# Kernel optimization log

Hardware: AMD Instinct MI355X
Metric: run time of the kernel (lower is better)

Reference implementation:

```python
import jax, jax.numpy as jnp
import numpy as np

D_MODEL = 1024
N_HEADS = 16
HEAD_DIM = D_MODEL // N_HEADS
FFN = 4096
NUM_REL = 64
BATCH = 4
SEQ = 1024
EPS = 1e-6


def _layernorm(x, g, b):
    mu = jnp.mean(x, axis=-1, keepdims=True)
    var = jnp.mean(jnp.square(x - mu), axis=-1, keepdims=True)
    return (x - mu) * jax.lax.rsqrt(var + EPS) * g + b


def setup_inputs() -> dict:
    key = jax.random.key(0)
    ks = jax.random.split(key, 16)
    s_d = 1.0 / np.sqrt(D_MODEL)
    s_f = 1.0 / np.sqrt(FFN)
    inp = {
        "x": jax.random.normal(ks[0], (BATCH, SEQ, D_MODEL), jnp.float32),
        "relative_ids": jax.random.randint(ks[1], (SEQ, SEQ), 0, NUM_REL),
        # attention projections (row-major: y = x @ W + b)
        "Wq": jax.random.normal(ks[2], (D_MODEL, D_MODEL), jnp.float32) * s_d,
        "bq": jnp.zeros((D_MODEL,), jnp.float32),
        "Wk": jax.random.normal(ks[3], (D_MODEL, D_MODEL), jnp.float32) * s_d,
        "bk": jnp.zeros((D_MODEL,), jnp.float32),
        "Wv": jax.random.normal(ks[4], (D_MODEL, D_MODEL), jnp.float32) * s_d,
        "bv": jnp.zeros((D_MODEL,), jnp.float32),
        "Wo": jax.random.normal(ks[5], (D_MODEL, D_MODEL), jnp.float32) * s_d,
        "bo": jnp.zeros((D_MODEL,), jnp.float32),
        # relative position tables: Ek for keys (rel-e), Eb per-head bias (rel-b)
        "Ek": jax.random.normal(ks[6], (NUM_REL, HEAD_DIM), jnp.float32) * (1.0 / np.sqrt(HEAD_DIM)),
        "Eb": jax.random.normal(ks[7], (NUM_REL, N_HEADS), jnp.float32) * 0.02,
        # layernorms
        "g1": jnp.ones((D_MODEL,), jnp.float32),
        "b1": jnp.zeros((D_MODEL,), jnp.float32),
        "g2": jnp.ones((D_MODEL,), jnp.float32),
        "b2": jnp.zeros((D_MODEL,), jnp.float32),
        # FFN
        "W1": jax.random.normal(ks[8], (D_MODEL, FFN), jnp.float32) * s_d,
        "bf1": jnp.zeros((FFN,), jnp.float32),
        "W2": jax.random.normal(ks[9], (FFN, D_MODEL), jnp.float32) * s_f,
        "bf2": jnp.zeros((D_MODEL,), jnp.float32),
    }
    return inp


def _forward(x, relative_ids, Wq, bq, Wk, bk, Wv, bv, Wo, bo, Ek, Eb,
             g1, b1, g2, b2, W1, bf1, W2, bf2):
    B, S, D = x.shape
    # projections -> [B, H, S, Dh]
    def split_heads(t):
        return t.reshape(B, S, N_HEADS, HEAD_DIM).transpose(0, 2, 1, 3)
    q = split_heads(x @ Wq + bq)
    k = split_heads(x @ Wk + bk)
    v = split_heads(x @ Wv + bv)

    scores = jnp.einsum('bhqd,bhkd->bhqk', q, k)
    # rel-e: relative key embeddings interact with queries
    Erel = Ek[relative_ids]                      # [S, S, Dh]
    scores = scores + jnp.einsum('bhqd,qkd->bhqk', q, Erel)
    # rel-b: per-head relative bias
    scores = scores + Eb[relative_ids].transpose(2, 0, 1)[None]  # [1,H,S,S]
    scores = scores / jnp.sqrt(jnp.asarray(HEAD_DIM, x.dtype))

    attn = jax.nn.softmax(scores, axis=-1)
    ctx = jnp.einsum('bhqk,bhkd->bhqd', attn, v)
    ctx = ctx.transpose(0, 2, 1, 3).reshape(B, S, D)
    a_out = ctx @ Wo + bo

    # dropout is identity at eval
    ff_in = _layernorm(x + a_out, g1, b1)
    ff = jax.nn.relu(ff_in @ W1 + bf1) @ W2 + bf2
    return _layernorm(ff_in + ff, g2, b2)


def reference(x, relative_ids, Wq, bq, Wk, bk, Wv, bv, Wo, bo, Ek, Eb,
              g1, b1, g2, b2, W1, bf1, W2, bf2):
    return _forward(x, relative_ids, Wq, bq, Wk, bk, Wv, bv, Wo, bo, Ek, Eb,
                    g1, b1, g2, b2, W1, bf1, W2, bf2)
```

## Files before the change

kernel.cpp:

```cpp
#include <hip/hip_runtime.h>


typedef short bf16x8 __attribute__((ext_vector_type(8)));
typedef float f32x4 __attribute__((ext_vector_type(4)));

#define DEVI static __device__ __forceinline__

constexpr int SEQ = 1024, DMODEL = 1024, NH = 16, HDIM = 64, FFDIM = 4096, NREL = 64, NBATCH = 4;
constexpr int ROWS = NBATCH * SEQ;
#define QSC 0.18033688011112042f
#define MAXC 16.0f

DEVI unsigned short f2b(float f) {
  union { float f; unsigned u; } v; v.f = f;
  unsigned r = v.u + 0x7FFFu + ((v.u >> 16) & 1u);
  return (unsigned short)(r >> 16);
}

#if __has_builtin(__builtin_amdgcn_cvt_pk_bf16_f32)
DEVI unsigned pack2(float a, float b) {
  auto r = __builtin_amdgcn_cvt_pk_bf16_f32(a, b);
  return __builtin_bit_cast(unsigned, r);
}
#else
DEVI unsigned pack2(float a, float b) {
  return (unsigned)f2b(a) | ((unsigned)f2b(b) << 16);
}
#endif

DEVI float fexp2(float x) {
#if __has_builtin(__builtin_amdgcn_exp2f)
  return __builtin_amdgcn_exp2f(x);
#else
  return exp2f(x);
#endif
}

DEVI void gload16(const unsigned short* g, unsigned short* l) {
  __builtin_amdgcn_global_load_lds((const __attribute__((address_space(1))) void*)g,
                                   (__attribute__((address_space(3))) void*)l, 16, 0, 0);
}

template <int BM, int BN, int WR, int WC>
DEVI void gemm_core(const unsigned short* __restrict__ A, int lda,
                    const unsigned short* __restrict__ Bt, int ldb, int K,
                    unsigned short* sA, unsigned short* sB, f32x4* acc) {
  constexpr int BK = 64;
  constexpr int MT = BM / (WR * 16), NT = BN / (WC * 16);
  const int tid = threadIdx.x;
  const int wave = tid >> 6, lane = tid & 63;
  const int wm = wave % WR, wn = wave / WR;
  const int lr = lane & 15, kq = lane >> 4;
  const int srow = lane >> 3;
  const int schunk = (lane & 7) ^ (srow & 7);
  const int sw = lr & 7;

  const f32x4 zero = {0.f, 0.f, 0.f, 0.f};
#pragma unroll
  for (int i = 0; i < MT * NT; ++i) acc[i] = zero;

  const unsigned short* ga = A + (size_t)(wave * (BM / 4) + srow) * lda + schunk * 8;
  const unsigned short* gb = Bt + (size_t)(wave * (BN / 4) + srow) * ldb + schunk * 8;
  unsigned short* la = sA + wave * (BM / 4) * BK;
  unsigned short* lb = sB + wave * (BN / 4) * BK;
  const unsigned short* pa = sA + (wm * MT * 16 + lr) * BK;
  const unsigned short* pb = sB + (wn * NT * 16 + lr) * BK;

  for (int k0 = 0; k0 < K; k0 += BK) {
#pragma unroll
    for (int j = 0; j < BM / 32; ++j) gload16(ga + (size_t)(j * 8) * lda + k0, la + j * 8 * BK);
#pragma unroll
    for (int j = 0; j < BN / 32; ++j) gload16(gb + (size_t)(j * 8) * ldb + k0, lb + j * 8 * BK);
    __syncthreads();
#pragma unroll
    for (int ks = 0; ks < 2; ++ks) {
      const int rc = ((ks * 4 + kq) ^ sw) * 8;
      bf16x8 af[MT], bv[NT];
#pragma unroll
      for (int mi = 0; mi < MT; ++mi) af[mi] = *(const bf16x8*)(pa + mi * 16 * BK + rc);
#pragma unroll
      for (int ni = 0; ni < NT; ++ni) bv[ni] = *(const bf16x8*)(pb + ni * 16 * BK + rc);
#pragma unroll
      for (int mi = 0; mi < MT; ++mi)
#pragma unroll
        for (int ni = 0; ni < NT; ++ni)
          acc[mi * NT + ni] =
              __builtin_amdgcn_mfma_f32_16x16x32_bf16(af[mi], bv[ni], acc[mi * NT + ni], 0, 0, 0);
    }
    __syncthreads();
  }
}

#define EPI_VARS                                     \
  const int tid = threadIdx.x;                       \
  const int wave = tid >> 6, lane = tid & 63;        \
  const int wm = wave % WR, wn = wave / WR;          \
  const int lr = lane & 15, kq = lane >> 4;

__global__ __launch_bounds__(256) void k_proj_qkv(
    const unsigned short* __restrict__ A, const unsigned short* __restrict__ WqT,
    const unsigned short* __restrict__ WkT, const unsigned short* __restrict__ WvT,
    const float* __restrict__ bq, const float* __restrict__ bk, const float* __restrict__ bv,
    unsigned short* __restrict__ oq, unsigned short* __restrict__ ok,
    unsigned short* __restrict__ ov) {
  constexpr int BM = 64, BN = 128, WR = 2, WC = 2, MT = 2, NT = 4;
  __shared__ __align__(16) unsigned short sA[BM * 64];
  __shared__ __align__(16) unsigned short sB[BN * 64];
  f32x4 acc[MT * NT];
  const int which = blockIdx.z;
  const unsigned short* Bt = which == 0 ? WqT : which == 1 ? WkT : WvT;
  const float* bias = which == 0 ? bq : which == 1 ? bk : bv;
  unsigned short* out = which == 0 ? oq : which == 1 ? ok : ov;
  const float scl = which == 0 ? QSC : 1.0f;
  const int m0 = blockIdx.y * BM, n0 = blockIdx.x * BN;
  gemm_core<BM, BN, WR, WC>(A + (size_t)m0 * DMODEL, DMODEL, Bt + (size_t)n0 * DMODEL, DMODEL,
                            DMODEL, sA, sB, acc);
  EPI_VARS
#pragma unroll
  for (int mi = 0; mi < MT; ++mi) {
    const int row0 = m0 + wm * MT * 16 + mi * 16 + kq * 4;
    const int b = row0 >> 10, s0 = row0 & 1023;
#pragma unroll
    for (int ni = 0; ni < NT; ++ni) {
      const int col = n0 + wn * NT * 16 + ni * 16 + lr;
      const int h = col >> 6, d = col & 63;
      const float bc = bias[col];
      f32x4 v = acc[mi * NT + ni];
#pragma unroll
      for (int r = 0; r < 4; ++r) v[r] = (v[r] + bc) * scl;
      if (which != 2) {
#pragma unroll
        for (int r = 0; r < 4; ++r)
          out[((size_t)((b * NH + h) * SEQ) + s0 + r) * HDIM + d] = f2b(v[r]);
      } else {
        uint2 p = make_uint2(pack2(v[0], v[1]), pack2(v[2], v[3]));
        *(uint2*)&out[((size_t)((b * NH + h) * HDIM) + d) * SEQ + s0] = p;
      }
    }
  }
}

template <int BM, int BN, int WR, int WC, bool RELU, bool OUTBF16>
__global__ __launch_bounds__(256) void k_gemm(const unsigned short* __restrict__ A, int lda,
                                              const unsigned short* __restrict__ Bt, int ldb, int K,
                                              int N, const float* __restrict__ bias,
                                              float* __restrict__ outf,
                                              unsigned short* __restrict__ outh) {
  constexpr int MT = BM / (WR * 16), NT = BN / (WC * 16);
  __shared__ __align__(16) unsigned short sA[BM * 64];
  __shared__ __align__(16) unsigned short sB[BN * 64];
  f32x4 acc[MT * NT];
  const int m0 = blockIdx.y * BM, n0 = blockIdx.x * BN;
  gemm_core<BM, BN, WR, WC>(A + (size_t)m0 * lda, lda, Bt + (size_t)n0 * ldb, ldb, K, sA, sB, acc);
  EPI_VARS
#pragma unroll
  for (int mi = 0; mi < MT; ++mi) {
    const int row0 = m0 + wm * MT * 16 + mi * 16 + kq * 4;
#pragma unroll
    for (int ni = 0; ni < NT; ++ni) {
      const int col = n0 + wn * NT * 16 + ni * 16 + lr;
      const float bc = bias ? bias[col] : 0.f;
      f32x4 v = acc[mi * NT + ni];
#pragma unroll
      for (int r = 0; r < 4; ++r) {
        float y = v[r] + bc;
        if (RELU) y = fmaxf(y, 0.f);
        if (OUTBF16)
          outh[(size_t)(row0 + r) * N + col] = f2b(y);
        else
          outf[(size_t)(row0 + r) * N + col] = y;
      }
    }
  }
}

__global__ __launch_bounds__(256) void k_flash(const unsigned short* __restrict__ q,
                                               const unsigned short* __restrict__ kk,
                                               const unsigned short* __restrict__ vT,
                                               const unsigned short* __restrict__ Ekb,
                                               const float* __restrict__ Eb,
                                               const int* __restrict__ rel,
                                               unsigned short* __restrict__ ctx) {
  __shared__ __align__(16) unsigned short sK[128 * 64];
  __shared__ __align__(16) unsigned short sV[64 * 128];
  __shared__ __align__(16) unsigned short sP[4][16 * 128];
  __shared__ __align__(16) float sqEB[64 * 68];
  __shared__ float sRow[4][16];

  const int tid = threadIdx.x, wave = tid >> 6, lane = tid & 63;
  const int lr = lane & 15, kq = lane >> 4;
  const int qt = blockIdx.x, z = blockIdx.y;
  const int b = z >> 4, h = z & 15;
  const size_t zo = (size_t)z * SEQ * HDIM;
  const size_t vo = (size_t)z * HDIM * SEQ;

  const int srow8 = lane >> 3, sl8 = lane & 7;
  const int sw8 = sl8 ^ (srow8 & 7);
  const int dl = lane >> 4, sl16 = lane & 15;
  const int swl = lr & 7;
  const f32x4 zero = {0.f, 0.f, 0.f, 0.f};

  unsigned short* sQv = &sP[0][0];
#pragma unroll
  for (int j = 0; j < 2; ++j) {
    const int row = wave * 16 + j * 8 + srow8;
    gload16(q + zo + (size_t)(qt * 64 + row) * 64 + sw8 * 8, sQv + (wave * 16 + j * 8) * 64);
    gload16(Ekb + (size_t)row * 64 + sw8 * 8, sK + (wave * 16 + j * 8) * 64);
  }
  __syncthreads();

  bf16x8 bq_[2];
#pragma unroll
  for (int ks = 0; ks < 2; ++ks)
    bq_[ks] = *(const bf16x8*)&sQv[(wave * 16 + lr) * 64 + (((ks * 4 + kq) ^ swl) << 3)];

  {
    f32x4 accE[4];
#pragma unroll
    for (int nf = 0; nf < 4; ++nf) accE[nf] = zero;
#pragma unroll
    for (int ks = 0; ks < 2; ++ks) {
#pragma unroll
      for (int nf = 0; nf < 4; ++nf) {
        bf16x8 ek = *(const bf16x8*)&sK[(nf * 16 + lr) * 64 + (((ks * 4 + kq) ^ swl) << 3)];
        accE[nf] = __builtin_amdgcn_mfma_f32_16x16x32_bf16(bq_[ks], ek, accE[nf], 0, 0, 0);
      }
    }
#pragma unroll
    for (int nf = 0; nf < 4; ++nf) {
      const int rid = nf * 16 + lr;
      const float eb = Eb[rid * NH + h] * QSC - MAXC;
      f32x4 vv = accE[nf];
      vv[0] += eb; vv[1] += eb; vv[2] += eb; vv[3] += eb;
      *(f32x4*)&sqEB[rid * 68 + wave * 16 + kq * 4] = vv;
    }
  }

  float l_run = 0.f;
  f32x4 accO[4];
#pragma unroll
  for (int nd = 0; nd < 4; ++nd) accO[nd] = zero;
  const int qrow_g = qt * 64 + wave * 16 + lr;
  const int* relrow = rel + (size_t)qrow_g * SEQ;
  const int qcol = wave * 16 + lr;
  unsigned short* sPw = sP[wave];

  for (int kt = 0; kt < 8; ++kt) {
    __syncthreads();
#pragma unroll
    for (int j = 0; j < 4; ++j) {
      const int row = wave * 32 + j * 8 + srow8;
      gload16(kk + zo + (size_t)(kt * 128 + row) * 64 + sw8 * 8, sK + (wave * 32 + j * 8) * 64);
    }
#pragma unroll
    for (int j = 0; j < 4; ++j) {
      const int row = wave * 16 + j * 4 + dl;
      const int ch = sl16 ^ (row & 15);
      gload16(vT + vo + (size_t)row * SEQ + kt * 128 + ch * 8, sV + (wave * 16 + j * 4) * 128);
    }
    int4 r4[8];
#pragma unroll
    for (int mi = 0; mi < 8; ++mi) r4[mi] = *(const int4*)&relrow[kt * 128 + mi * 16 + kq * 4];
    __syncthreads();

    f32x4 accS[8];
#pragma unroll
    for (int mi = 0; mi < 8; ++mi) accS[mi] = zero;
#pragma unroll
    for (int ks = 0; ks < 2; ++ks) {
#pragma unroll
      for (int mi = 0; mi < 8; ++mi) {
        bf16x8 a = *(const bf16x8*)&sK[(mi * 16 + lr) * 64 + (((ks * 4 + kq) ^ swl) << 3)];
        accS[mi] = __builtin_amdgcn_mfma_f32_16x16x32_bf16(a, bq_[ks], accS[mi], 0, 0, 0);
      }
    }
#pragma unroll
    for (int mi = 0; mi < 8; ++mi) {
      const float p0 = fexp2(accS[mi][0] + sqEB[r4[mi].x * 68 + qcol]);
      const float p1 = fexp2(accS[mi][1] + sqEB[r4[mi].y * 68 + qcol]);
      const float p2 = fexp2(accS[mi][2] + sqEB[r4[mi].z * 68 + qcol]);
      const float p3 = fexp2(accS[mi][3] + sqEB[r4[mi].w * 68 + qcol]);
      accS[mi][0] = p0; accS[mi][1] = p1; accS[mi][2] = p2; accS[mi][3] = p3;
      l_run += (p0 + p1) + (p2 + p3);
    }
#pragma unroll
    for (int mi = 0; mi < 8; ++mi) {
      const int c = 2 * mi + (kq >> 1);
      *(uint2*)&sPw[lr * 128 + ((c ^ lr) << 3) + ((kq & 1) << 2)] =
          make_uint2(pack2(accS[mi][0], accS[mi][1]), pack2(accS[mi][2], accS[mi][3]));
    }
#pragma unroll
    for (int kst = 0; kst < 4; ++kst) {
      const int cc = ((kq + 4 * kst) ^ lr) << 3;
      bf16x8 a = *(const bf16x8*)&sPw[lr * 128 + cc];
#pragma unroll
      for (int nd = 0; nd < 4; ++nd) {
        bf16x8 bv = *(const bf16x8*)&sV[(nd * 16 + lr) * 128 + cc];
        accO[nd] = __builtin_amdgcn_mfma_f32_16x16x32_bf16(a, bv, accO[nd], 0, 0, 0);
      }
    }
  }

  l_run += __shfl_xor(l_run, 16);
  l_run += __shfl_xor(l_run, 32);
  if (kq == 0) sRow[wave][lr] = l_run;
  const float4 lv = *(const float4*)&sRow[wave][kq * 4];
  const float inv[4] = {1.f / lv.x, 1.f / lv.y, 1.f / lv.z, 1.f / lv.w};
  const size_t rbase = (size_t)(b * SEQ + qt * 64 + wave * 16 + kq * 4);
#pragma unroll
  for (int nd = 0; nd < 4; ++nd) {
    const int col = h * HDIM + nd * 16 + lr;
#pragma unroll
    for (int r = 0; r < 4; ++r)
      ctx[(rbase + r) * DMODEL + col] = f2b(accO[nd][r] * inv[r]);
  }
}

template <bool WB>
__global__ __launch_bounds__(256) void k_addln(const float* __restrict__ a,
                                               const float* __restrict__ b,
                                               const float* __restrict__ g,
                                               const float* __restrict__ beta,
                                               float* __restrict__ outf,
                                               unsigned short* __restrict__ outh) {
  const int row = blockIdx.x, t = threadIdx.x;
  const size_t base = (size_t)row * DMODEL + t * 4;
  float4 va = *(const float4*)&a[base];
  float4 vb = *(const float4*)&b[base];
  const float x0 = va.x + vb.x, x1 = va.y + vb.y, x2 = va.z + vb.z, x3 = va.w + vb.w;
  __shared__ float red[4];
  float s = x0 + x1 + x2 + x3;
#pragma unroll
  for (int o = 32; o; o >>= 1) s += __shfl_xor(s, o);
  if ((t & 63) == 0) red[t >> 6] = s;
  __syncthreads();
  const float mu = (red[0] + red[1] + red[2] + red[3]) * (1.0f / DMODEL);
  __syncthreads();
  const float d0 = x0 - mu, d1 = x1 - mu, d2 = x2 - mu, d3 = x3 - mu;
  float qv = d0 * d0 + d1 * d1 + d2 * d2 + d3 * d3;
#pragma unroll
  for (int o = 32; o; o >>= 1) qv += __shfl_xor(qv, o);
  if ((t & 63) == 0) red[t >> 6] = qv;
  __syncthreads();
  const float var = (red[0] + red[1] + red[2] + red[3]) * (1.0f / DMODEL);
  const float sc = rsqrtf(var + 1e-6f);
  float4 vg = *(const float4*)&g[t * 4];
  float4 ve = *(const float4*)&beta[t * 4];
  float4 y;
  y.x = d0 * sc * vg.x + ve.x;
  y.y = d1 * sc * vg.y + ve.y;
  y.z = d2 * sc * vg.z + ve.z;
  y.w = d3 * sc * vg.w + ve.w;
  *(float4*)&outf[base] = y;
  if (WB) {
    uint2 p = make_uint2(pack2(y.x, y.y), pack2(y.z, y.w));
    *(uint2*)&outh[base] = p;
  }
}

DEVI void tcast_body(const float* in, unsigned short* out, int R, int C) {
  __shared__ float tile[32][33];
  const int tx = threadIdx.x & 31, ty = threadIdx.x >> 5;
  const int r0 = blockIdx.y * 32, c0 = blockIdx.x * 32;
#pragma unroll
  for (int i = 0; i < 4; ++i) tile[ty + i * 8][tx] = in[(size_t)(r0 + ty + i * 8) * C + c0 + tx];
  __syncthreads();
#pragma unroll
  for (int i = 0; i < 4; ++i)
    out[(size_t)(c0 + ty + i * 8) * R + r0 + tx] = f2b(tile[tx][ty + i * 8]);
}

__global__ __launch_bounds__(256) void k_tcast(const float* __restrict__ in,
                                               unsigned short* __restrict__ out, int R, int C) {
  tcast_body(in, out, R, C);
}

__global__ __launch_bounds__(256) void k_tcast4(const float* __restrict__ w0,
                                                const float* __restrict__ w1,
                                                const float* __restrict__ w2,
                                                const float* __restrict__ w3,
                                                unsigned short* __restrict__ o0,
                                                unsigned short* __restrict__ o1,
                                                unsigned short* __restrict__ o2,
                                                unsigned short* __restrict__ o3) {
  const int zz = blockIdx.z;
  const float* in = zz == 0 ? w0 : zz == 1 ? w1 : zz == 2 ? w2 : w3;
  unsigned short* out = zz == 0 ? o0 : zz == 1 ? o1 : zz == 2 ? o2 : o3;
  tcast_body(in, out, DMODEL, DMODEL);
}

__global__ __launch_bounds__(256) void k_cast2(const float* __restrict__ a,
                                               unsigned short* __restrict__ oa, int n4a,
                                               const float* __restrict__ bsrc,
                                               unsigned short* __restrict__ ob, int n4b) {
  const int i = blockIdx.x * 256 + threadIdx.x;
  if (i < n4a) {
    float4 v = *(const float4*)&a[(size_t)i * 4];
    uint2 p = make_uint2(pack2(v.x, v.y), pack2(v.z, v.w));
    *(uint2*)&oa[(size_t)i * 4] = p;
  } else {
    const int j = i - n4a;
    if (j < n4b) {
      float4 v = *(const float4*)&bsrc[(size_t)j * 4];
      uint2 p = make_uint2(pack2(v.x, v.y), pack2(v.z, v.w));
      *(uint2*)&ob[(size_t)j * 4] = p;
    }
  }
}


extern "C" void kernel_launch(void* const* d_in, const int* in_sizes, int n_in, void* d_out,
                              int out_size, void* d_ws, size_t ws_size, hipStream_t stream) {
  const float* x = (const float*)d_in[0];
  const int* rel = (const int*)d_in[1];
  const float* Wq = (const float*)d_in[2];
  const float* bq = (const float*)d_in[3];
  const float* Wk = (const float*)d_in[4];
  const float* bk = (const float*)d_in[5];
  const float* Wv = (const float*)d_in[6];
  const float* bv = (const float*)d_in[7];
  const float* Wo = (const float*)d_in[8];
  const float* bo = (const float*)d_in[9];
  const float* Ek = (const float*)d_in[10];
  const float* Eb = (const float*)d_in[11];
  const float* g1 = (const float*)d_in[12];
  const float* b1 = (const float*)d_in[13];
  const float* g2 = (const float*)d_in[14];
  const float* b2 = (const float*)d_in[15];
  const float* W1 = (const float*)d_in[16];
  const float* bf1 = (const float*)d_in[17];
  const float* W2 = (const float*)d_in[18];
  const float* bf2 = (const float*)d_in[19];
  float* out = (float*)d_out;

  char* ws = (char*)d_ws;
  const size_t MB = 1ull << 20;
  unsigned short* Wqt = (unsigned short*)(ws + 0 * MB);
  unsigned short* Wkt = (unsigned short*)(ws + 2 * MB);
  unsigned short* Wvt = (unsigned short*)(ws + 4 * MB);
  unsigned short* Wot = (unsigned short*)(ws + 6 * MB);
  unsigned short* W1t = (unsigned short*)(ws + 8 * MB);
  unsigned short* W2t = (unsigned short*)(ws + 16 * MB);
  unsigned short* xb = (unsigned short*)(ws + 24 * MB);
  unsigned short* Ekb = (unsigned short*)(ws + 32 * MB);
  unsigned short* qbuf = (unsigned short*)(ws + 33 * MB);
  unsigned short* kbuf = (unsigned short*)(ws + 41 * MB);
  unsigned short* vTb = (unsigned short*)(ws + 49 * MB);
  unsigned short* ctx = (unsigned short*)(ws + 73 * MB);
  float* a_out = (float*)(ws + 81 * MB);
  float* ff_in = (float*)(ws + 97 * MB);
  unsigned short* ff_in_b = (unsigned short*)(ws + 113 * MB);
  unsigned short* hidden = (unsigned short*)(ws + 121 * MB);
  float* ffo = (float*)(ws + 153 * MB);

  k_tcast4<<<dim3(32, 32, 4), 256, 0, stream>>>(Wq, Wk, Wv, Wo, Wqt, Wkt, Wvt, Wot);
  k_tcast<<<dim3(128, 32), 256, 0, stream>>>(W1, W1t, DMODEL, FFDIM);
  k_tcast<<<dim3(32, 128), 256, 0, stream>>>(W2, W2t, FFDIM, DMODEL);
  k_cast2<<<4100, 256, 0, stream>>>(x, xb, ROWS * DMODEL / 4, Ek, Ekb, NREL * HDIM / 4);

  k_proj_qkv<<<dim3(8, 64, 3), 256, 0, stream>>>(xb, Wqt, Wkt, Wvt, bq, bk, bv, qbuf, kbuf, vTb);

  k_flash<<<dim3(16, 64), 256, 0, stream>>>(qbuf, kbuf, vTb, Ekb, Eb, rel, ctx);

  k_gemm<64, 128, 2, 2, false, false><<<dim3(8, 64), 256, 0, stream>>>(
      ctx, DMODEL, Wot, DMODEL, DMODEL, DMODEL, bo, a_out, nullptr);
  k_addln<true><<<ROWS, 256, 0, stream>>>(x, a_out, g1, b1, ff_in, ff_in_b);

  k_gemm<128, 128, 2, 2, true, true><<<dim3(32, 32), 256, 0, stream>>>(
      ff_in_b, DMODEL, W1t, DMODEL, DMODEL, FFDIM, bf1, nullptr, hidden);
  k_gemm<64, 128, 2, 2, false, false><<<dim3(8, 64), 256, 0, stream>>>(
      hidden, FFDIM, W2t, FFDIM, FFDIM, DMODEL, bf2, ffo, nullptr);

  k_addln<false><<<ROWS, 256, 0, stream>>>(ff_in, ffo, g2, b2, out, nullptr);
}
```

Baseline: 407.2 us.

## Enlarge GEMM tiles, split-K Wo/W2 with fused partial-sum LayerNorm, V from registers

The QKV projection tile grows from 64 to 128 rows. The Wo and W2 GEMMs now use 128x128 tiles with a two-way split-K. The two fp32 partial outputs are summed inside the add+LayerNorm kernel, which now reads three inputs. In the flash kernel, V fragments are loaded straight from global memory into registers instead of being staged through shared memory, which frees LDS and removes those stores. The trade-offs are extra partial-buffer traffic, more registers per thread, and uncoalesced direct V loads.

Result: slower. 429.5 us (+5.5%).

```diff
diff --git a/kernel.cpp b/kernel.cpp
--- a/kernel.cpp
+++ b/kernel.cpp
@@ -103,7 +103,7 @@
     const float* __restrict__ bq, const float* __restrict__ bk, const float* __restrict__ bv,
     unsigned short* __restrict__ oq, unsigned short* __restrict__ ok,
     unsigned short* __restrict__ ov) {
-  constexpr int BM = 64, BN = 128, WR = 2, WC = 2, MT = 2, NT = 4;
+  constexpr int BM = 128, BN = 128, WR = 2, WC = 2, MT = 4, NT = 4;
   __shared__ __align__(16) unsigned short sA[BM * 64];
   __shared__ __align__(16) unsigned short sB[BN * 64];
   f32x4 acc[MT * NT];
@@ -140,18 +140,22 @@
   }
 }
 
-template <int BM, int BN, int WR, int WC, bool RELU, bool OUTBF16>
+template <int BM, int BN, int WR, int WC, bool RELU, bool OUTBF16, bool SPLITK = false>
 __global__ __launch_bounds__(256) void k_gemm(const unsigned short* __restrict__ A, int lda,
                                               const unsigned short* __restrict__ Bt, int ldb, int K,
                                               int N, const float* __restrict__ bias,
                                               float* __restrict__ outf,
-                                              unsigned short* __restrict__ outh) {
+                                              unsigned short* __restrict__ outh,
+                                              size_t ostride = 0) {
   constexpr int MT = BM / (WR * 16), NT = BN / (WC * 16);
   __shared__ __align__(16) unsigned short sA[BM * 64];
   __shared__ __align__(16) unsigned short sB[BN * 64];
   f32x4 acc[MT * NT];
   const int m0 = blockIdx.y * BM, n0 = blockIdx.x * BN;
-  gemm_core<BM, BN, WR, WC>(A + (size_t)m0 * lda, lda, Bt + (size_t)n0 * ldb, ldb, K, sA, sB, acc);
+  const int kc = SPLITK ? blockIdx.z : 0;
+  gemm_core<BM, BN, WR, WC>(A + (size_t)m0 * lda + (size_t)kc * K, lda,
+                            Bt + (size_t)n0 * ldb + (size_t)kc * K, ldb, K, sA, sB, acc);
+  if (SPLITK) outf += (size_t)kc * ostride;
   EPI_VARS
 #pragma unroll
   for (int mi = 0; mi < MT; ++mi) {
@@ -159,7 +163,7 @@
 #pragma unroll
     for (int ni = 0; ni < NT; ++ni) {
       const int col = n0 + wn * NT * 16 + ni * 16 + lr;
-      const float bc = bias ? bias[col] : 0.f;
+      const float bc = (bias && (!SPLITK || kc == 0)) ? bias[col] : 0.f;
       f32x4 v = acc[mi * NT + ni];
 #pragma unroll
       for (int r = 0; r < 4; ++r) {
@@ -182,7 +186,6 @@
                                                const int* __restrict__ rel,
                                                unsigned short* __restrict__ ctx) {
   __shared__ __align__(16) unsigned short sK[128 * 64];
-  __shared__ __align__(16) unsigned short sV[64 * 128];
   __shared__ __align__(16) unsigned short sP[4][16 * 128];
   __shared__ __align__(16) float sqEB[64 * 68];
   __shared__ float sRow[4][16];
@@ -196,7 +199,6 @@
 
   const int srow8 = lane >> 3, sl8 = lane & 7;
   const int sw8 = sl8 ^ (srow8 & 7);
-  const int dl = lane >> 4, sl16 = lane & 15;
   const int swl = lr & 7;
   const f32x4 zero = {0.f, 0.f, 0.f, 0.f};
 
@@ -244,6 +246,9 @@
   const int* relrow = rel + (size_t)qrow_g * SEQ;
   const int qcol = wave * 16 + lr;
   unsigned short* sPw = sP[wave];
+  const unsigned short* vrow[4];
+#pragma unroll
+  for (int nd = 0; nd < 4; ++nd) vrow[nd] = vT + vo + (size_t)(nd * 16 + lr) * SEQ + kq * 8;
 
   for (int kt = 0; kt < 8; ++kt) {
     __syncthreads();
@@ -252,12 +257,12 @@
       const int row = wave * 32 + j * 8 + srow8;
       gload16(kk + zo + (size_t)(kt * 128 + row) * 64 + sw8 * 8, sK + (wave * 32 + j * 8) * 64);
     }
-#pragma unroll
-    for (int j = 0; j < 4; ++j) {
-      const int row = wave * 16 + j * 4 + dl;
-      const int ch = sl16 ^ (row & 15);
-      gload16(vT + vo + (size_t)row * SEQ + kt * 128 + ch * 8, sV + (wave * 16 + j * 4) * 128);
-    }
+    bf16x8 bvv[4][4];
+#pragma unroll
+    for (int kst = 0; kst < 2; ++kst)
+#pragma unroll
+      for (int nd = 0; nd < 4; ++nd)
+        bvv[kst][nd] = *(const bf16x8*)(vrow[nd] + kt * 128 + kst * 32);
     int4 r4[8];
 #pragma unroll
     for (int mi = 0; mi < 8; ++mi) r4[mi] = *(const int4*)&relrow[kt * 128 + mi * 16 + kq * 4];
@@ -283,6 +288,12 @@
       accS[mi][0] = p0; accS[mi][1] = p1; accS[mi][2] = p2; accS[mi][3] = p3;
       l_run += (p0 + p1) + (p2 + p3);
     }
+    bf16x8 bvv2[2][4];
+#pragma unroll
+    for (int kst = 0; kst < 2; ++kst)
+#pragma unroll
+      for (int nd = 0; nd < 4; ++nd)
+        bvv2[kst][nd] = *(const bf16x8*)(vrow[nd] + kt * 128 + (kst + 2) * 32);
 #pragma unroll
     for (int mi = 0; mi < 8; ++mi) {
       const int c = 2 * mi + (kq >> 1);
@@ -295,7 +306,7 @@
       bf16x8 a = *(const bf16x8*)&sPw[lr * 128 + cc];
 #pragma unroll
       for (int nd = 0; nd < 4; ++nd) {
-        bf16x8 bv = *(const bf16x8*)&sV[(nd * 16 + lr) * 128 + cc];
+        bf16x8 bv = kst < 2 ? bvv[kst][nd] : bvv2[kst - 2][nd];
         accO[nd] = __builtin_amdgcn_mfma_f32_16x16x32_bf16(a, bv, accO[nd], 0, 0, 0);
       }
     }
@@ -317,17 +328,20 @@
 }
 
 template <bool WB>
-__global__ __launch_bounds__(256) void k_addln(const float* __restrict__ a,
-                                               const float* __restrict__ b,
-                                               const float* __restrict__ g,
-                                               const float* __restrict__ beta,
-                                               float* __restrict__ outf,
-                                               unsigned short* __restrict__ outh) {
+__global__ __launch_bounds__(256) void k_addln3(const float* __restrict__ a,
+                                                const float* __restrict__ p0,
+                                                const float* __restrict__ p1,
+                                                const float* __restrict__ g,
+                                                const float* __restrict__ beta,
+                                                float* __restrict__ outf,
+                                                unsigned short* __restrict__ outh) {
   const int row = blockIdx.x, t = threadIdx.x;
   const size_t base = (size_t)row * DMODEL + t * 4;
   float4 va = *(const float4*)&a[base];
-  float4 vb = *(const float4*)&b[base];
-  const float x0 = va.x + vb.x, x1 = va.y + vb.y, x2 = va.z + vb.z, x3 = va.w + vb.w;
+  float4 v0 = *(const float4*)&p0[base];
+  float4 v1 = *(const float4*)&p1[base];
+  const float x0 = va.x + v0.x + v1.x, x1 = va.y + v0.y + v1.y;
+  const float x2 = va.z + v0.z + v1.z, x3 = va.w + v0.w + v1.w;
   __shared__ float red[4];
   float s = x0 + x1 + x2 + x3;
 #pragma unroll
@@ -447,29 +461,29 @@
   unsigned short* kbuf = (unsigned short*)(ws + 41 * MB);
   unsigned short* vTb = (unsigned short*)(ws + 49 * MB);
   unsigned short* ctx = (unsigned short*)(ws + 73 * MB);
-  float* a_out = (float*)(ws + 81 * MB);
-  float* ff_in = (float*)(ws + 97 * MB);
-  unsigned short* ff_in_b = (unsigned short*)(ws + 113 * MB);
-  unsigned short* hidden = (unsigned short*)(ws + 121 * MB);
-  float* ffo = (float*)(ws + 153 * MB);
+  float* P0 = (float*)(ws + 81 * MB);
+  float* P1 = (float*)(ws + 97 * MB);
+  float* ff_in = (float*)(ws + 113 * MB);
+  unsigned short* ff_in_b = (unsigned short*)(ws + 129 * MB);
+  unsigned short* hidden = (unsigned short*)(ws + 137 * MB);
+  const size_t OST = (size_t)ROWS * DMODEL;
 
   k_tcast4<<<dim3(32, 32, 4), 256, 0, stream>>>(Wq, Wk, Wv, Wo, Wqt, Wkt, Wvt, Wot);
   k_tcast<<<dim3(128, 32), 256, 0, stream>>>(W1, W1t, DMODEL, FFDIM);
   k_tcast<<<dim3(32, 128), 256, 0, stream>>>(W2, W2t, FFDIM, DMODEL);
   k_cast2<<<4100, 256, 0, stream>>>(x, xb, ROWS * DMODEL / 4, Ek, Ekb, NREL * HDIM / 4);
 
-  k_proj_qkv<<<dim3(8, 64, 3), 256, 0, stream>>>(xb, Wqt, Wkt, Wvt, bq, bk, bv, qbuf, kbuf, vTb);
+  k_proj_qkv<<<dim3(8, 32, 3), 256, 0, stream>>>(xb, Wqt, Wkt, Wvt, bq, bk, bv, qbuf, kbuf, vTb);
 
   k_flash<<<dim3(16, 64), 256, 0, stream>>>(qbuf, kbuf, vTb, Ekb, Eb, rel, ctx);
 
-  k_gemm<64, 128, 2, 2, false, false><<<dim3(8, 64), 256, 0, stream>>>(
-      ctx, DMODEL, Wot, DMODEL, DMODEL, DMODEL, bo, a_out, nullptr);
-  k_addln<true><<<ROWS, 256, 0, stream>>>(x, a_out, g1, b1, ff_in, ff_in_b);
+  k_gemm<128, 128, 2, 2, false, false, true><<<dim3(8, 32, 2), 256, 0, stream>>>(
+      ctx, DMODEL, Wot, DMODEL, DMODEL / 2, DMODEL, bo, P0, nullptr, OST);
+  k_addln3<true><<<ROWS, 256, 0, stream>>>(x, P0, P1, g1, b1, ff_in, ff_in_b);
 
   k_gemm<128, 128, 2, 2, true, true><<<dim3(32, 32), 256, 0, stream>>>(
       ff_in_b, DMODEL, W1t, DMODEL, DMODEL, FFDIM, bf1, nullptr, hidden);
-  k_gemm<64, 128, 2, 2, false, false><<<dim3(8, 64), 256, 0, stream>>>(
-      hidden, FFDIM, W2t, FFDIM, FFDIM, DMODEL, bf2, ffo, nullptr);
-
-  k_addln<false><<<ROWS, 256, 0, stream>>>(ff_in, ffo, g2, b2, out, nullptr);
-}
+  k_gemm<128, 128, 2, 2, false, false, true><<<dim3(8, 32, 2), 256, 0, stream>>>(
+      hidden, FFDIM, W2t, FFDIM, FFDIM / 2, DMODEL, bf2, P0, nullptr, OST);
+  k_addln3<false><<<ROWS, 256, 0, stream>>>(ff_in, P0, P1, g2, b2, out, nullptr);
+}
```

## Split-K bf16 partials for output GEMMs, merge weight casts, shrink flash LDS

Applied to the files above, without the earlier changes.

Several changes land together. The Wo and W2 GEMMs move to 128x128 tiles with a 2-way split-K that writes bf16 partials, and a three-input add+layernorm kernel sums them. The residual path now reads bf16 copies of x and ff_in instead of fp32, which removes fp32 intermediates and the fp32 ff_in buffer. The six weight transpose-casts are merged into one launch, the QKV projection uses larger tiles, and the flash kernel reuses sK/sV as scratch for P and Q, with an extra barrier, to cut LDS use. Rounding the residual and the partial sums to bf16 lowers precision.

New measurement: 380.9 us. 6.5% less time.

```diff
diff --git a/kernel.cpp b/kernel.cpp
--- a/kernel.cpp
+++ b/kernel.cpp
@@ -34,6 +34,13 @@
 #else
   return exp2f(x);
 #endif
+}
+
+DEVI float4 ld4h(const unsigned short* p) {
+  uint2 u = *(const uint2*)p;
+  union { unsigned v; float f; } a, b, c, d;
+  a.v = u.x << 16; b.v = u.x & 0xffff0000u; c.v = u.y << 16; d.v = u.y & 0xffff0000u;
+  return make_float4(a.f, b.f, c.f, d.f);
 }
 
 DEVI void gload16(const unsigned short* g, unsigned short* l) {
@@ -103,7 +110,7 @@
     const float* __restrict__ bq, const float* __restrict__ bk, const float* __restrict__ bv,
     unsigned short* __restrict__ oq, unsigned short* __restrict__ ok,
     unsigned short* __restrict__ ov) {
-  constexpr int BM = 64, BN = 128, WR = 2, WC = 2, MT = 2, NT = 4;
+  constexpr int BM = 128, BN = 128, WR = 2, WC = 2, MT = 4, NT = 4;
   __shared__ __align__(16) unsigned short sA[BM * 64];
   __shared__ __align__(16) unsigned short sB[BN * 64];
   f32x4 acc[MT * NT];
@@ -140,18 +147,22 @@
   }
 }
 
-template <int BM, int BN, int WR, int WC, bool RELU, bool OUTBF16>
+template <int BM, int BN, int WR, int WC, bool RELU, bool OUTBF16, bool SPLITK = false>
 __global__ __launch_bounds__(256) void k_gemm(const unsigned short* __restrict__ A, int lda,
                                               const unsigned short* __restrict__ Bt, int ldb, int K,
                                               int N, const float* __restrict__ bias,
                                               float* __restrict__ outf,
-                                              unsigned short* __restrict__ outh) {
+                                              unsigned short* __restrict__ outh,
+                                              size_t ostride = 0) {
   constexpr int MT = BM / (WR * 16), NT = BN / (WC * 16);
   __shared__ __align__(16) unsigned short sA[BM * 64];
   __shared__ __align__(16) unsigned short sB[BN * 64];
   f32x4 acc[MT * NT];
   const int m0 = blockIdx.y * BM, n0 = blockIdx.x * BN;
-  gemm_core<BM, BN, WR, WC>(A + (size_t)m0 * lda, lda, Bt + (size_t)n0 * ldb, ldb, K, sA, sB, acc);
+  const int kc = SPLITK ? blockIdx.z : 0;
+  gemm_core<BM, BN, WR, WC>(A + (size_t)m0 * lda + (size_t)kc * K, lda,
+                            Bt + (size_t)n0 * ldb + (size_t)kc * K, ldb, K, sA, sB, acc);
+  if (SPLITK) outh += (size_t)kc * ostride;
   EPI_VARS
 #pragma unroll
   for (int mi = 0; mi < MT; ++mi) {
@@ -159,13 +170,13 @@
 #pragma unroll
     for (int ni = 0; ni < NT; ++ni) {
       const int col = n0 + wn * NT * 16 + ni * 16 + lr;
-      const float bc = bias ? bias[col] : 0.f;
+      const float bc = (bias && (!SPLITK || kc == 0)) ? bias[col] : 0.f;
       f32x4 v = acc[mi * NT + ni];
 #pragma unroll
       for (int r = 0; r < 4; ++r) {
         float y = v[r] + bc;
         if (RELU) y = fmaxf(y, 0.f);
-        if (OUTBF16)
+        if (OUTBF16 || SPLITK)
           outh[(size_t)(row0 + r) * N + col] = f2b(y);
         else
           outf[(size_t)(row0 + r) * N + col] = y;
@@ -183,7 +194,6 @@
                                                unsigned short* __restrict__ ctx) {
   __shared__ __align__(16) unsigned short sK[128 * 64];
   __shared__ __align__(16) unsigned short sV[64 * 128];
-  __shared__ __align__(16) unsigned short sP[4][16 * 128];
   __shared__ __align__(16) float sqEB[64 * 68];
   __shared__ float sRow[4][16];
 
@@ -200,7 +210,7 @@
   const int swl = lr & 7;
   const f32x4 zero = {0.f, 0.f, 0.f, 0.f};
 
-  unsigned short* sQv = &sP[0][0];
+  unsigned short* sQv = sV;
 #pragma unroll
   for (int j = 0; j < 2; ++j) {
     const int row = wave * 16 + j * 8 + srow8;
@@ -243,7 +253,7 @@
   const int qrow_g = qt * 64 + wave * 16 + lr;
   const int* relrow = rel + (size_t)qrow_g * SEQ;
   const int qcol = wave * 16 + lr;
-  unsigned short* sPw = sP[wave];
+  unsigned short* sPw = sK + wave * 2048;
 
   for (int kt = 0; kt < 8; ++kt) {
     __syncthreads();
@@ -283,6 +293,8 @@
       accS[mi][0] = p0; accS[mi][1] = p1; accS[mi][2] = p2; accS[mi][3] = p3;
       l_run += (p0 + p1) + (p2 + p3);
     }
+    __syncthreads();
+
 #pragma unroll
     for (int mi = 0; mi < 8; ++mi) {
       const int c = 2 * mi + (kq >> 1);
@@ -317,17 +329,20 @@
 }
 
 template <bool WB>
-__global__ __launch_bounds__(256) void k_addln(const float* __restrict__ a,
-                                               const float* __restrict__ b,
-                                               const float* __restrict__ g,
-                                               const float* __restrict__ beta,
-                                               float* __restrict__ outf,
-                                               unsigned short* __restrict__ outh) {
+__global__ __launch_bounds__(256) void k_addln3(const unsigned short* __restrict__ a,
+                                                const unsigned short* __restrict__ p0,
+                                                const unsigned short* __restrict__ p1,
+                                                const float* __restrict__ g,
+                                                const float* __restrict__ beta,
+                                                float* __restrict__ outf,
+                                                unsigned short* __restrict__ outh) {
   const int row = blockIdx.x, t = threadIdx.x;
   const size_t base = (size_t)row * DMODEL + t * 4;
-  float4 va = *(const float4*)&a[base];
-  float4 vb = *(const float4*)&b[base];
-  const float x0 = va.x + vb.x, x1 = va.y + vb.y, x2 = va.z + vb.z, x3 = va.w + vb.w;
+  float4 va = ld4h(&a[base]);
+  float4 v0 = ld4h(&p0[base]);
+  float4 v1 = ld4h(&p1[base]);
+  const float x0 = va.x + v0.x + v1.x, x1 = va.y + v0.y + v1.y;
+  const float x2 = va.z + v0.z + v1.z, x3 = va.w + v0.w + v1.w;
   __shared__ float red[4];
   float s = x0 + x1 + x2 + x3;
 #pragma unroll
@@ -351,42 +366,47 @@
   y.y = d1 * sc * vg.y + ve.y;
   y.z = d2 * sc * vg.z + ve.z;
   y.w = d3 * sc * vg.w + ve.w;
-  *(float4*)&outf[base] = y;
   if (WB) {
     uint2 p = make_uint2(pack2(y.x, y.y), pack2(y.z, y.w));
     *(uint2*)&outh[base] = p;
-  }
-}
-
-DEVI void tcast_body(const float* in, unsigned short* out, int R, int C) {
+  } else {
+    *(float4*)&outf[base] = y;
+  }
+}
+
+__global__ __launch_bounds__(256) void k_tcast12(
+    const float* __restrict__ Wq, const float* __restrict__ Wk, const float* __restrict__ Wv,
+    const float* __restrict__ Wo, const float* __restrict__ W1, const float* __restrict__ W2,
+    unsigned short* __restrict__ oq, unsigned short* __restrict__ ok,
+    unsigned short* __restrict__ ov, unsigned short* __restrict__ oo,
+    unsigned short* __restrict__ o1, unsigned short* __restrict__ o2) {
+  const int z = blockIdx.z;
+  const float* in;
+  unsigned short* out;
+  int ldi, ldo;
+  if (z < 4) {
+    in = z == 0 ? Wq : z == 1 ? Wk : z == 2 ? Wv : Wo;
+    out = z == 0 ? oq : z == 1 ? ok : z == 2 ? ov : oo;
+    ldi = 1024; ldo = 1024;
+  } else if (z < 8) {
+    const int s = z - 4;
+    in = W1 + (size_t)s * 1024; ldi = 4096;
+    out = o1 + (size_t)s * 1024 * 1024; ldo = 1024;
+  } else {
+    const int s = z - 8;
+    in = W2 + (size_t)s * 1024 * 1024; ldi = 1024;
+    out = o2 + (size_t)s * 1024; ldo = 4096;
+  }
   __shared__ float tile[32][33];
   const int tx = threadIdx.x & 31, ty = threadIdx.x >> 5;
   const int r0 = blockIdx.y * 32, c0 = blockIdx.x * 32;
 #pragma unroll
-  for (int i = 0; i < 4; ++i) tile[ty + i * 8][tx] = in[(size_t)(r0 + ty + i * 8) * C + c0 + tx];
+  for (int i = 0; i < 4; ++i)
+    tile[ty + i * 8][tx] = in[(size_t)(r0 + ty + i * 8) * ldi + c0 + tx];
   __syncthreads();
 #pragma unroll
   for (int i = 0; i < 4; ++i)
-    out[(size_t)(c0 + ty + i * 8) * R + r0 + tx] = f2b(tile[tx][ty + i * 8]);
-}
-
-__global__ __launch_bounds__(256) void k_tcast(const float* __restrict__ in,
-                                               unsigned short* __restrict__ out, int R, int C) {
-  tcast_body(in, out, R, C);
-}
-
-__global__ __launch_bounds__(256) void k_tcast4(const float* __restrict__ w0,
-                                                const float* __restrict__ w1,
-                                                const float* __restrict__ w2,
-                                                const float* __restrict__ w3,
-                                                unsigned short* __restrict__ o0,
-                                                unsigned short* __restrict__ o1,
-                                                unsigned short* __restrict__ o2,
-                                                unsigned short* __restrict__ o3) {
-  const int zz = blockIdx.z;
-  const float* in = zz == 0 ? w0 : zz == 1 ? w1 : zz == 2 ? w2 : w3;
-  unsigned short* out = zz == 0 ? o0 : zz == 1 ? o1 : zz == 2 ? o2 : o3;
-  tcast_body(in, out, DMODEL, DMODEL);
+    out[(size_t)(c0 + ty + i * 8) * ldo + r0 + tx] = f2b(tile[tx][ty + i * 8]);
 }
 
 __global__ __launch_bounds__(256) void k_cast2(const float* __restrict__ a,
@@ -446,30 +466,27 @@
   unsigned short* qbuf = (unsigned short*)(ws + 33 * MB);
   unsigned short* kbuf = (unsigned short*)(ws + 41 * MB);
   unsigned short* vTb = (unsigned short*)(ws + 49 * MB);
-  unsigned short* ctx = (unsigned short*)(ws + 73 * MB);
-  float* a_out = (float*)(ws + 81 * MB);
-  float* ff_in = (float*)(ws + 97 * MB);
-  unsigned short* ff_in_b = (unsigned short*)(ws + 113 * MB);
-  unsigned short* hidden = (unsigned short*)(ws + 121 * MB);
-  float* ffo = (float*)(ws + 153 * MB);
-
-  k_tcast4<<<dim3(32, 32, 4), 256, 0, stream>>>(Wq, Wk, Wv, Wo, Wqt, Wkt, Wvt, Wot);
-  k_tcast<<<dim3(128, 32), 256, 0, stream>>>(W1, W1t, DMODEL, FFDIM);
-  k_tcast<<<dim3(32, 128), 256, 0, stream>>>(W2, W2t, FFDIM, DMODEL);
+  unsigned short* ctx = (unsigned short*)(ws + 57 * MB);
+  unsigned short* Pb = (unsigned short*)(ws + 65 * MB);
+  unsigned short* ff_in_b = (unsigned short*)(ws + 81 * MB);
+  unsigned short* hidden = (unsigned short*)(ws + 89 * MB);
+  const size_t OST = (size_t)ROWS * DMODEL;
+
+  k_tcast12<<<dim3(32, 32, 12), 256, 0, stream>>>(Wq, Wk, Wv, Wo, W1, W2, Wqt, Wkt, Wvt, Wot,
+                                                  W1t, W2t);
   k_cast2<<<4100, 256, 0, stream>>>(x, xb, ROWS * DMODEL / 4, Ek, Ekb, NREL * HDIM / 4);
 
-  k_proj_qkv<<<dim3(8, 64, 3), 256, 0, stream>>>(xb, Wqt, Wkt, Wvt, bq, bk, bv, qbuf, kbuf, vTb);
+  k_proj_qkv<<<dim3(8, 32, 3), 256, 0, stream>>>(xb, Wqt, Wkt, Wvt, bq, bk, bv, qbuf, kbuf, vTb);
 
   k_flash<<<dim3(16, 64), 256, 0, stream>>>(qbuf, kbuf, vTb, Ekb, Eb, rel, ctx);
 
-  k_gemm<64, 128, 2, 2, false, false><<<dim3(8, 64), 256, 0, stream>>>(
-      ctx, DMODEL, Wot, DMODEL, DMODEL, DMODEL, bo, a_out, nullptr);
-  k_addln<true><<<ROWS, 256, 0, stream>>>(x, a_out, g1, b1, ff_in, ff_in_b);
+  k_gemm<128, 128, 2, 2, false, true, true><<<dim3(8, 32, 2), 256, 0, stream>>>(
+      ctx, DMODEL, Wot, DMODEL, DMODEL / 2, DMODEL, bo, nullptr, Pb, OST);
+  k_addln3<true><<<ROWS, 256, 0, stream>>>(xb, Pb, Pb + OST, g1, b1, nullptr, ff_in_b);
 
   k_gemm<128, 128, 2, 2, true, true><<<dim3(32, 32), 256, 0, stream>>>(
       ff_in_b, DMODEL, W1t, DMODEL, DMODEL, FFDIM, bf1, nullptr, hidden);
-  k_gemm<64, 128, 2, 2, false, false><<<dim3(8, 64), 256, 0, stream>>>(
-      hidden, FFDIM, W2t, FFDIM, FFDIM, DMODEL, bf2, ffo, nullptr);
-
-  k_addln<false><<<ROWS, 256, 0, stream>>>(ff_in, ffo, g2, b2, out, nullptr);
-}
+  k_gemm<128, 128, 2, 2, false, true, true><<<dim3(8, 32, 2), 256, 0, stream>>>(
+      hidden, FFDIM, W2t, FFDIM, FFDIM / 2, DMODEL, bf2, nullptr, Pb, OST);
+  k_addln3<false><<<ROWS, 256, 0, stream>>>(ff_in_b, Pb, Pb + OST, g2, b2, out, nullptr);
+}
```
